# Kernel tuning notes

Hardware: AMD Instinct MI355X
Metric: run time of the kernel (lower is better)

Reference implementation:

```python
import jax, jax.numpy as jnp
import numpy as np

B, S, D = 4, 1024, 2048
H, KVH, HD = 32, 8, 64
N_REP = H // KVH  # 4
ROPE_THETA = 1000000.0


def _rope_tables(seq_len, head_dim, theta):
    inv_freq = 1.0 / (theta ** (np.arange(0, head_dim, 2, dtype=np.float32) / head_dim))
    t = np.arange(seq_len, dtype=np.float32)
    freqs = np.outer(t, inv_freq)                      # (S, HD/2)
    emb = np.concatenate([freqs, freqs], axis=-1)      # (S, HD)
    return jnp.asarray(np.cos(emb)), jnp.asarray(np.sin(emb))


def setup_inputs() -> dict:
    key = jax.random.key(0)
    kx, kq, kk, kv, ko = jax.random.split(key, 5)
    cos, sin = _rope_tables(S, HD, ROPE_THETA)
    s = 0.02
    return {
        "x": jax.random.normal(kx, (B, S, D), jnp.float32),
        "cos": cos,
        "sin": sin,
        "Wq": jax.random.normal(kq, (D, H * HD), jnp.float32) * s,
        "Wk": jax.random.normal(kk, (D, KVH * HD), jnp.float32) * s,
        "Wv": jax.random.normal(kv, (D, KVH * HD), jnp.float32) * s,
        "Wo": jax.random.normal(ko, (H * HD, D), jnp.float32) * s,
    }


def _rotate_half(t):
    t1, t2 = jnp.split(t, 2, axis=-1)
    return jnp.concatenate([-t2, t1], axis=-1)


def reference(x, cos, sin, Wq, Wk, Wv, Wo):
    # projections
    q = (x @ Wq).reshape(B, S, H, HD)      # (b, s, h, d)
    k = (x @ Wk).reshape(B, S, KVH, HD)
    v = (x @ Wv).reshape(B, S, KVH, HD)

    # RoPE: cos/sin (s, d) broadcast over heads (unsqueeze_dim=1 -> (s,1,d))
    c = cos[:, None, :]
    sn = sin[:, None, :]
    q = q * c + _rotate_half(q) * sn
    k = k * c + _rotate_half(k) * sn

    # GQA attention without physically repeating KV:
    # q grouped as (b, kvh, n_rep, s, d); repeat_kv '(h r)' maps q head g*n_rep+r -> kv head g
    qg = q.transpose(0, 2, 1, 3).reshape(B, KVH, N_REP, S, HD)
    kt = k.transpose(0, 2, 1, 3)  # (b, kvh, s, d)
    vt = v.transpose(0, 2, 1, 3)

    scale = 1.0 / jnp.sqrt(jnp.asarray(HD, x.dtype))
    scores = jnp.einsum('bgrqd,bgkd->bgrqk', qg, kt) * scale  # (b, kvh, rep, s, s)
    probs = jax.nn.softmax(scores, axis=-1)
    out = jnp.einsum('bgrqk,bgkd->bgrqd', probs, vt)           # (b, kvh, rep, s, d)

    out = out.reshape(B, H, S, HD).transpose(0, 2, 1, 3).reshape(B, S, H * HD)
    return out @ Wo
```

## Files before the change

### kernel.cpp

```cpp
#include <hip/hip_runtime.h>

typedef unsigned short u16;
typedef __attribute__((ext_vector_type(8))) __bf16 bf16x8;
typedef __attribute__((ext_vector_type(4))) _Float16 f16x4;
typedef __attribute__((ext_vector_type(8))) _Float16 f16x8;
typedef __attribute__((ext_vector_type(4))) float f32x4;

#define BB 4
#define SS 1024
#define DD 2048
#define HH 32
#define KVHN 8
#define HDIM 64

__device__ __forceinline__ u16 f2b(float f) {
    union { float f; unsigned u; } v; v.f = f;
    unsigned r = v.u + 0x7FFFu + ((v.u >> 16) & 1u);
    return (u16)(r >> 16);
}
__device__ __forceinline__ float b2f(u16 h) {
    union { unsigned u; float f; } v; v.u = ((unsigned)h) << 16; return v.f;
}

__device__ __forceinline__ f32x4 mfma16(bf16x8 a, bf16x8 b, f32x4 c) {
    return __builtin_amdgcn_mfma_f32_16x16x32_bf16(a, b, c, 0, 0, 0);
}
__device__ __forceinline__ f32x4 mfma16h(f16x8 a, f16x8 b, f32x4 c) {
    return __builtin_amdgcn_mfma_f32_16x16x32_f16(a, b, c, 0, 0, 0);
}

__device__ __forceinline__ void async_cp16(const void* g, void* l) {
    __builtin_amdgcn_global_load_lds((__attribute__((address_space(1))) void*)g,
                                     (__attribute__((address_space(3))) void*)l,
                                     16, 0, 0);
}

__device__ __forceinline__ void block_sync() {
    asm volatile("" ::: "memory");
    __builtin_amdgcn_s_barrier();
    asm volatile("" ::: "memory");
}

__device__ __forceinline__ f16x8 pack8_f16(const float* p) {
    union { unsigned u[4]; f16x8 v; } pu;
    pu.u[0] = __builtin_bit_cast(unsigned, __builtin_amdgcn_cvt_pkrtz(p[0], p[1]));
    pu.u[1] = __builtin_bit_cast(unsigned, __builtin_amdgcn_cvt_pkrtz(p[2], p[3]));
    pu.u[2] = __builtin_bit_cast(unsigned, __builtin_amdgcn_cvt_pkrtz(p[4], p[5]));
    pu.u[3] = __builtin_bit_cast(unsigned, __builtin_amdgcn_cvt_pkrtz(p[6], p[7]));
    return pu.v;
}

__global__ __launch_bounds__(256) void prep_kernel(const float* __restrict__ x,
                                                   const float* __restrict__ Wq,
                                                   const float* __restrict__ Wk,
                                                   const float* __restrict__ Wv,
                                                   const float* __restrict__ Wo,
                                                   u16* __restrict__ xb,
                                                   u16* __restrict__ Wqkvt,
                                                   u16* __restrict__ Wot) {
    __shared__ float tile[32][33];
    int z = blockIdx.z;
    int tid = threadIdx.x;
    if (z == 4) {
        int lb = blockIdx.y * 64 + blockIdx.x;
        int i = (lb * 256 + tid) * 8;
        float4 v0 = *(const float4*)(x + i);
        float4 v1 = *(const float4*)(x + i + 4);
        uint4 r;
        r.x = (unsigned)f2b(v0.x) | ((unsigned)f2b(v0.y) << 16);
        r.y = (unsigned)f2b(v0.z) | ((unsigned)f2b(v0.w) << 16);
        r.z = (unsigned)f2b(v1.x) | ((unsigned)f2b(v1.y) << 16);
        r.w = (unsigned)f2b(v1.z) | ((unsigned)f2b(v1.w) << 16);
        *(uint4*)(xb + i) = r;
        return;
    }
    const float* W = (z == 0) ? Wq : (z == 1) ? Wk : (z == 2) ? Wv : Wo;
    int N = (z == 1 || z == 2) ? 512 : 2048;
    int n_off = (z == 1) ? 2048 : (z == 2) ? 2560 : 0;
    u16* Wt = (z == 3) ? Wot : Wqkvt;
    int n0 = blockIdx.x * 32;
    if (n0 >= N) return;
    int k0 = blockIdx.y * 32;
    int nj = tid & 31;
    int ki = tid >> 5;
#pragma unroll
    for (int it = 0; it < 4; it++) {
        int kk = it * 8 + ki;
        tile[kk][nj] = W[(size_t)(k0 + kk) * N + n0 + nj];
    }
    __syncthreads();
#pragma unroll
    for (int it = 0; it < 4; it++) {
        int nn = it * 8 + ki;
        Wt[(size_t)(n0 + nn + n_off) * 2048 + k0 + nj] = f2b(tile[nj][nn]);
    }
}

__global__ __launch_bounds__(512, 2) void gemm_qkv(const u16* __restrict__ A,
                                                   const u16* __restrict__ Bt,
                                                   u16* __restrict__ C) {
    __shared__ __align__(16) u16 Ls[2][32768];
    const int tid = threadIdx.x;
    const int lane = tid & 63;
    const int w = tid >> 6;

    const int bid = blockIdx.x;
    const int xcd = bid & 7;
    const int loc = bid >> 3;
    const int mt = (xcd & 3) * 4 + (loc & 3);
    const int nt = (xcd >> 2) * 6 + (loc >> 2);
    const int m0 = mt * 256;
    const int n0 = nt * 256;

    const int wm_h = w >> 2;
    const int wn = (w & 3) * 64;
    const int lr = lane & 15;
    const int lg = lane >> 4;

    const int sr = lane >> 3;
    const int sl = (lane & 7) ^ (sr & 7);
    const u16* pA = A + (size_t)(m0 + w * 8 + sr) * 2048 + sl * 8;
    const u16* pB = Bt + (size_t)(n0 + w * 8 + sr) * 2048 + sl * 8;

#define STA(buf_, h_, kt_)                                                               \
    {                                                                                    \
        async_cp16(pA + (size_t)((h_) * 128) * 2048 + (kt_) * 64, &Ls[buf_][(h_) * 8192 + w * 512]);            \
        async_cp16(pA + (size_t)((h_) * 128 + 64) * 2048 + (kt_) * 64, &Ls[buf_][(h_) * 8192 + 4096 + w * 512]); \
    }
#define STB(buf_, h_, kt_)                                                               \
    {                                                                                    \
        async_cp16(pB + (size_t)((h_) * 128) * 2048 + (kt_) * 64, &Ls[buf_][16384 + (h_) * 8192 + w * 512]);            \
        async_cp16(pB + (size_t)((h_) * 128 + 64) * 2048 + (kt_) * 64, &Ls[buf_][16384 + (h_) * 8192 + 4096 + w * 512]); \
    }

    f32x4 acc[8][4];
    const f32x4 zero4 = {0.f, 0.f, 0.f, 0.f};
#pragma unroll
    for (int i = 0; i < 8; i++)
#pragma unroll
        for (int j = 0; j < 4; j++) acc[i][j] = zero4;

    bf16x8 af[8], b0[4], b1[4];

#define LDA(mh_, buf_)                                                                   \
    _Pragma("unroll") for (int mi = 0; mi < 4; mi++) _Pragma("unroll") for (int ks = 0; ks < 2; ks++) { \
        int rh = (mh_) * 64 + mi * 16 + lr;                                              \
        af[mi * 2 + ks] = *(const bf16x8*)(&Ls[buf_][wm_h * 8192 + rh * 64 + (((ks * 4 + lg) ^ (lr & 7)) * 8)]); \
    }
#define LDB(dst_, nh_, buf_)                                                             \
    _Pragma("unroll") for (int ni = 0; ni < 2; ni++) _Pragma("unroll") for (int ks = 0; ks < 2; ks++) { \
        int rowb = wn + (nh_) * 32 + ni * 16 + lr;                                       \
        dst_[ni * 2 + ks] = *(const bf16x8*)(&Ls[buf_][16384 + (rowb >> 7) * 8192 + (rowb & 127) * 64 + (((ks * 4 + lg) ^ (lr & 7)) * 8)]); \
    }
#define QMM(mh_, nh_, bb_)                                                               \
    __builtin_amdgcn_s_setprio(1);                                                       \
    _Pragma("unroll") for (int mi = 0; mi < 4; mi++) _Pragma("unroll") for (int ni = 0; ni < 2; ni++) { \
        acc[(mh_) * 4 + mi][(nh_) * 2 + ni] = mfma16(af[mi * 2 + 0], bb_[ni * 2 + 0], acc[(mh_) * 4 + mi][(nh_) * 2 + ni]); \
        acc[(mh_) * 4 + mi][(nh_) * 2 + ni] = mfma16(af[mi * 2 + 1], bb_[ni * 2 + 1], acc[(mh_) * 4 + mi][(nh_) * 2 + ni]); \
    }                                                                                    \
    __builtin_amdgcn_s_setprio(0);
#define WAITLDS                                                                          \
    asm volatile("s_waitcnt lgkmcnt(0)" ::: "memory");                                   \
    __builtin_amdgcn_sched_barrier(0);

    STA(0, 0, 0); STA(0, 1, 0); STB(0, 0, 0); STB(0, 1, 0);
    STB(1, 0, 1); STB(1, 1, 1);
    asm volatile("s_waitcnt vmcnt(0)" ::: "memory");
    block_sync();

#pragma unroll 1
    for (int I = 0; I < 16; ++I) {
        const int tb = 2 * I + 1;
        const int ta2 = (2 * I + 2) & 31;
        const int tb2 = (2 * I + 3) & 31;

        LDA(0, 0); LDB(b0, 0, 0);
        STA(1, 0, tb);
        block_sync(); WAITLDS;
        QMM(0, 0, b0);
        block_sync();

        LDB(b1, 1, 0);
        STA(1, 1, tb);
        block_sync(); WAITLDS;
        QMM(0, 1, b1);
        block_sync();

        LDA(1, 0);
        STB(0, 0, ta2);
        block_sync(); WAITLDS;
        QMM(1, 1, b1);
        block_sync();

        STB(0, 1, ta2);
        block_sync(); WAITLDS;
        QMM(1, 0, b0);
        asm volatile("s_waitcnt vmcnt(4)" ::: "memory");
        block_sync();

        LDA(0, 1); LDB(b0, 0, 1);
        STA(0, 0, ta2);
        block_sync(); WAITLDS;
        QMM(0, 0, b0);
        block_sync();

        LDB(b1, 1, 1);
        STA(0, 1, ta2);
        block_sync(); WAITLDS;
        QMM(0, 1, b1);
        block_sync();

        LDA(1, 1);
        STB(1, 0, tb2);
        block_sync(); WAITLDS;
        QMM(1, 1, b1);
        block_sync();

        STB(1, 1, tb2);
        block_sync(); WAITLDS;
        QMM(1, 0, b0);
        asm volatile("s_waitcnt vmcnt(4)" ::: "memory");
        block_sync();
    }
    asm volatile("s_waitcnt vmcnt(0)" ::: "memory");

    const int lq = lg * 4;
    const int wm = wm_h * 128;
#pragma unroll
    for (int mi = 0; mi < 8; mi++)
#pragma unroll
        for (int ni = 0; ni < 4; ni++)
#pragma unroll
            for (int i = 0; i < 4; i++) {
                int r = m0 + wm + mi * 16 + lq + i;
                int c = n0 + wn + ni * 16 + lr;
                C[(size_t)r * 3072 + c] = f2b(acc[mi][ni][i]);
            }
#undef STA
#undef STB
#undef LDA
#undef LDB
#undef QMM
#undef WAITLDS
}

__global__ __launch_bounds__(512, 2) void gemm_out(const u16* __restrict__ A,
                                                   const u16* __restrict__ Bt,
                                                   float* __restrict__ C) {
    __shared__ __align__(16) u16 Ls[2][24576];
    const int tid = threadIdx.x;
    const int lane = tid & 63;
    const int w = tid >> 6;

    const int bid = blockIdx.x;
    const int xcd = bid & 7;
    const int loc = bid >> 3;
    const int mt = (xcd & 3) * 4 + (loc & 3);
    const int nt = (xcd >> 2) * 8 + (loc >> 2);
    const int m0 = mt * 256;
    const int n0 = nt * 128;

    const int wm = (w >> 2) * 128;
    const int wn = (w & 3) * 32;
    const int lr = lane & 15;
    const int lg = lane >> 4;

    const int row0 = tid >> 2;
    const int g = tid & 3;
    const int sg = g ^ ((row0 >> 1) & 3);
    const u16* pA0 = A + (size_t)(m0 + row0) * 2048 + sg * 8;
    const u16* pA1 = pA0 + (size_t)128 * 2048;
    const u16* pB0 = Bt + (size_t)(n0 + row0) * 2048 + sg * 8;

#define OSTA(buf_, ks_, T_)                                                     \
    {                                                                           \
        async_cp16(pA0 + (T_) * 64 + (ks_) * 32, &Ls[buf_][(ks_) * 8192 + w * 512]);        \
        async_cp16(pA1 + (T_) * 64 + (ks_) * 32, &Ls[buf_][(ks_) * 8192 + 4096 + w * 512]); \
    }
#define OSTB(buf_, ks_, T_)                                                     \
    {                                                                           \
        async_cp16(pB0 + (T_) * 64 + (ks_) * 32, &Ls[buf_][16384 + (ks_) * 4096 + w * 512]); \
    }

    f32x4 acc[8][2];
    const f32x4 zero4 = {0.f, 0.f, 0.f, 0.f};
#pragma unroll
    for (int i = 0; i < 8; i++)
#pragma unroll
        for (int j = 0; j < 2; j++) acc[i][j] = zero4;

    bf16x8 af[8], bfr[2];

#define OLDA(ks_)                                                               \
    _Pragma("unroll") for (int mi = 0; mi < 8; mi++) {                          \
        int r_ = wm + mi * 16 + lr;                                             \
        af[mi] = *(const bf16x8*)(&Ls[cur][(ks_) * 8192 + r_ * 32 + ((lg ^ ((r_ >> 1) & 3)) * 8)]); \
    }
#define OLDB(ks_)                                                               \
    _Pragma("unroll") for (int ni = 0; ni < 2; ni++) {                          \
        int r_ = wn + ni * 16 + lr;                                             \
        bfr[ni] = *(const bf16x8*)(&Ls[cur][16384 + (ks_) * 4096 + r_ * 32 + ((lg ^ ((r_ >> 1) & 3)) * 8)]); \
    }
#define OMM                                                                     \
    __builtin_amdgcn_s_setprio(1);                                              \
    _Pragma("unroll") for (int mi = 0; mi < 8; mi++) _Pragma("unroll") for (int ni = 0; ni < 2; ni++) { \
        acc[mi][ni] = mfma16(af[mi], bfr[ni], acc[mi][ni]);                     \
    }                                                                           \
    __builtin_amdgcn_s_setprio(0);
#define OWAITMM                                                                 \
    asm volatile("s_waitcnt lgkmcnt(0)" ::: "memory");                          \
    __builtin_amdgcn_sched_barrier(0);

    OSTA(0, 0, 0); OSTB(0, 0, 0); OSTA(0, 1, 0); OSTB(0, 1, 0);
    OSTA(1, 0, 1); OSTB(1, 0, 1);
    asm volatile("s_waitcnt vmcnt(3)" ::: "memory");
    block_sync();

#pragma unroll 2
    for (int T = 0; T < 32; ++T) {
        const int cur = T & 1;
        const int oth = cur ^ 1;
        const int Tp1 = (T + 1) & 31;
        const int Tp2 = (T + 2) & 31;

        OLDA(0); OLDB(0);
        OSTA(oth, 1, Tp1); OSTB(oth, 1, Tp1);
        block_sync(); OWAITMM;
        OMM;
        block_sync();

        OLDA(1); OLDB(1);
        OSTA(cur, 0, Tp2); OSTB(cur, 0, Tp2);
        block_sync(); OWAITMM;
        OMM;
        asm volatile("s_waitcnt vmcnt(3)" ::: "memory");
        block_sync();
    }
    asm volatile("s_waitcnt vmcnt(0)" ::: "memory");

    const int lq = lg * 4;
#pragma unroll
    for (int mi = 0; mi < 8; mi++)
#pragma unroll
        for (int ni = 0; ni < 2; ni++)
#pragma unroll
            for (int i = 0; i < 4; i++) {
                int r = m0 + wm + mi * 16 + lq + i;
                int c = n0 + wn + ni * 16 + lr;
                C[(size_t)r * 2048 + c] = acc[mi][ni][i];
            }
#undef OSTA
#undef OSTB
#undef OLDA
#undef OLDB
#undef OMM
#undef OWAITMM
}

__global__ __launch_bounds__(256) void ropevt_kernel(const u16* __restrict__ QKV,
                                                     const float* __restrict__ cosT,
                                                     const float* __restrict__ sinT,
                                                     u16* __restrict__ Qh,
                                                     u16* __restrict__ Kh,
                                                     u16* __restrict__ Vt) {
    __shared__ u16 tile[64][65];
    const int bid = blockIdx.x;
    const int tid = threadIdx.x;
    if (bid < 20480) {
        const float QSC = 0.125f * 1.44269504088896f;
        int idx = bid * 256 + tid;
        int d = idx & 31;
        int t = idx >> 5;
        int hh = t % 40;
        int row = t / 40;
        int s = row & (SS - 1);
        int b = row >> 10;
        float c = cosT[s * HDIM + d];
        float sn = sinT[s * HDIM + d];
        if (hh < 32) {
            const u16* src = QKV + (size_t)row * 3072 + hh * 64 + d;
            float x1 = b2f(src[0]), x2 = b2f(src[32]);
            u16* dst = Qh + ((size_t)(b * HH + hh) * SS + s) * 64 + d;
            dst[0] = f2b((x1 * c - x2 * sn) * QSC);
            dst[32] = f2b((x2 * c + x1 * sn) * QSC);
        } else {
            int g = hh - 32;
            const u16* src = QKV + (size_t)row * 3072 + 2048 + g * 64 + d;
            float x1 = b2f(src[0]), x2 = b2f(src[32]);
            int rr = s & 7;
            int kpos = (s & ~31) + ((rr >= 4) ? 16 : 0) + ((s >> 3) & 3) * 4 + (rr & 3);
            u16* dst = Kh + ((size_t)(b * KVHN + g) * SS + kpos) * 64 + d;
            dst[0] = f2b(x1 * c - x2 * sn);
            dst[32] = f2b(x2 * c + x1 * sn);
        }
        return;
    }
    int blk = bid - 20480;
    int st = blk & 15;
    int t2 = blk >> 4;
    int g = t2 & 7;
    int b = t2 >> 3;
    int cj = tid & 63;
    int ri = tid >> 6;
    const u16* src = QKV + ((size_t)(b * SS + st * 64)) * 3072 + 2560 + g * 64;
#pragma unroll
    for (int it = 0; it < 16; it++) {
        int s_i = it * 4 + ri;
        tile[s_i][cj] = src[(size_t)s_i * 3072 + cj];
    }
    __syncthreads();
    u16* dst = Vt + ((size_t)(b * KVHN + g) * HDIM) * SS + st * 64;
#pragma unroll
    for (int it = 0; it < 16; it++) {
        int hd_i = it * 4 + ri;
        _Float16 hv = (_Float16)b2f(tile[cj][hd_i]);
        union { _Float16 h; u16 u; } cv; cv.h = hv;
        dst[(size_t)hd_i * SS + cj] = cv.u;
    }
}

__global__ __launch_bounds__(256, 2) void flash_kernel(const u16* __restrict__ Qh,
                                                       const u16* __restrict__ Kh,
                                                       const u16* __restrict__ Vt,
                                                       u16* __restrict__ Attn) {
    __shared__ __align__(16) u16 Kls[2][4096];
    __shared__ __align__(16) u16 Vls[2][4096];
    const int tid = threadIdx.x;
    const int lane = tid & 63;
    const int w = tid >> 6;
    const int bid = blockIdx.x;
    const int gbp = ((bid & 7) << 2) | ((bid >> 3) & 3);
    const int qt2 = bid >> 5;
    const int g = gbp & 7;
    const int b = gbp >> 3;
    const int h = g * 4 + w;
    const int lr = lane & 15;
    const int lg = lane >> 4;
    const int lk8 = lg * 8;
    const int lq = lg * 4;

    const u16* Qbase = Qh + ((size_t)(b * HH + h) * SS + qt2 * 64) * HDIM;
    bf16x8 qb[4][2];
#pragma unroll
    for (int j = 0; j < 4; j++) {
        qb[j][0] = *(const bf16x8*)(Qbase + (size_t)(j * 16 + lr) * HDIM + lk8);
        qb[j][1] = *(const bf16x8*)(Qbase + (size_t)(j * 16 + lr) * HDIM + 32 + lk8);
    }

    const u16* Kbase = Kh + (size_t)(b * KVHN + g) * SS * HDIM;
    const u16* Vbase = Vt + (size_t)(b * KVHN + g) * HDIM * SS;

    const int r0 = tid >> 3;
    const int c0 = tid & 7;

    const f32x4 zero4 = {0.f, 0.f, 0.f, 0.f};
    const f32x4 initS = {-4.f, -4.f, -4.f, -4.f};
    f32x4 o[4][4];
    float lsum[4] = {0.f, 0.f, 0.f, 0.f};
#pragma unroll
    for (int j = 0; j < 4; j++)
#pragma unroll
        for (int i = 0; i < 4; i++) o[j][i] = zero4;

#define STAGE(kt, p)                                                              \
    {                                                                             \
        _Pragma("unroll") for (int sh = 0; sh < 2; sh++) {                        \
            int rr = r0 + sh * 32;                                                \
            int cs = c0 ^ (rr & 7);                                              \
            async_cp16(Kbase + (size_t)((kt) + rr) * HDIM + cs * 8,               \
                       &Kls[p][sh * 2048 + w * 512]);                             \
            async_cp16(Vbase + (size_t)rr * SS + (kt) + cs * 8,                   \
                       &Vls[p][sh * 2048 + w * 512]);                             \
        }                                                                         \
    }

    STAGE(0, 0);
    __syncthreads();

    for (int t = 0; t < 16; t++) {
        const int p = t & 1;
        if (t < 15) STAGE((t + 1) * 64, p ^ 1);

#pragma unroll
        for (int c = 0; c < 2; c++) {
            f32x4 s[2][4];
#pragma unroll
            for (int halfi = 0; halfi < 2; halfi++) {
                const int R = c * 32 + halfi * 16 + lr;
                const u16* kr = &Kls[p][R * 64];
                bf16x8 kb0 = *(const bf16x8*)(kr + ((lg ^ (R & 7)) * 8));
                bf16x8 kb1 = *(const bf16x8*)(kr + (((4 + lg) ^ (R & 7)) * 8));
#pragma unroll
                for (int j = 0; j < 4; j++) {
                    f32x4 a = initS;
                    a = mfma16(kb0, qb[j][0], a);
                    a = mfma16(kb1, qb[j][1], a);
                    s[halfi][j] = a;
                }
            }

            f16x8 va[4];
#pragma unroll
            for (int hdt = 0; hdt < 4; hdt++) {
                const int R2 = hdt * 16 + lr;
                va[hdt] = *(const f16x8*)(&Vls[p][R2 * 64 + (((c * 4 + lg) ^ (R2 & 7)) * 8)]);
            }

#pragma unroll
            for (int j = 0; j < 4; j++) {
                float pv[8];
#pragma unroll
                for (int r = 0; r < 4; r++) {
                    pv[r] = __builtin_amdgcn_exp2f(s[0][j][r]);
                    pv[4 + r] = __builtin_amdgcn_exp2f(s[1][j][r]);
                }
                lsum[j] += ((pv[0] + pv[1]) + (pv[2] + pv[3])) +
                           ((pv[4] + pv[5]) + (pv[6] + pv[7]));
                f16x8 pb = pack8_f16(pv);
#pragma unroll
                for (int hdt = 0; hdt < 4; hdt++)
                    o[j][hdt] = mfma16h(va[hdt], pb, o[j][hdt]);
            }
        }
        __syncthreads();
    }

#pragma unroll
    for (int j = 0; j < 4; j++) {
        float su = lsum[j];
        su += __shfl_xor(su, 16);
        su += __shfl_xor(su, 32);
        float inv = 1.f / su;
        u16* Ob = Attn + ((size_t)(b * SS + qt2 * 64 + j * 16 + lr)) * 2048 + h * 64;
#pragma unroll
        for (int hdt = 0; hdt < 4; hdt++) {
            unsigned r0p = (unsigned)f2b(o[j][hdt][0] * inv) | ((unsigned)f2b(o[j][hdt][1] * inv) << 16);
            unsigned r1p = (unsigned)f2b(o[j][hdt][2] * inv) | ((unsigned)f2b(o[j][hdt][3] * inv) << 16);
            *(uint2*)(Ob + hdt * 16 + lq) = make_uint2(r0p, r1p);
        }
    }
}

extern "C" void kernel_launch(void* const* d_in, const int* in_sizes, int n_in,
                              void* d_out, int out_size, void* d_ws, size_t ws_size,
                              hipStream_t stream) {
    (void)in_sizes; (void)n_in; (void)out_size; (void)ws_size;
    const float* x = (const float*)d_in[0];
    const float* cosT = (const float*)d_in[1];
    const float* sinT = (const float*)d_in[2];
    const float* Wq = (const float*)d_in[3];
    const float* Wk = (const float*)d_in[4];
    const float* Wv = (const float*)d_in[5];
    const float* Wo = (const float*)d_in[6];
    float* out = (float*)d_out;

    char* ws = (char*)d_ws;
    u16* Xb    = (u16*)(ws);
    u16* Wqkvt = (u16*)(ws + 16777216);
    u16* Wot   = (u16*)(ws + 29360128);
    u16* QKV   = (u16*)(ws + 37748736);
    u16* Qh    = (u16*)(ws + 62914560);
    u16* Kh    = (u16*)(ws + 79691776);
    u16* Vt    = (u16*)(ws + 83886080);
    u16* Attn  = (u16*)(ws + 88080384);

    prep_kernel<<<dim3(64, 64, 5), 256, 0, stream>>>(x, Wq, Wk, Wv, Wo, Xb, Wqkvt, Wot);

    gemm_qkv<<<192, 512, 0, stream>>>(Xb, Wqkvt, QKV);

    ropevt_kernel<<<20992, 256, 0, stream>>>(QKV, cosT, sinT, Qh, Kh, Vt);

    flash_kernel<<<512, 256, 0, stream>>>(Qh, Kh, Vt, Attn);

    gemm_out<<<256, 512, 0, stream>>>(Attn, Wot, out);
}
```

Measured before the change: 258.5 us.

## Vectorize RoPE and weight-transpose stores, rebalance gemm_out warp tiling

The RoPE kernel now has each thread handle 8 contiguous elements with 16-byte loads and stores instead of scalar 2-byte accesses, which cuts its block count from 20480 to 2560. The weight transpose in prep packs two bf16 values into each 32-bit store. gemm_out's per-wave tile changes from 128x32 to 64x64, which lowers LDS fragment reads per MFMA (8 fragment loads for 16 MFMAs instead of 10). The goal is less memory-instruction overhead in the small kernels and better LDS reuse in the output GEMM.

```diff
diff --git a/kernel.cpp b/kernel.cpp
--- a/kernel.cpp
+++ b/kernel.cpp
@@ -89,10 +89,14 @@
         tile[kk][nj] = W[(size_t)(k0 + kk) * N + n0 + nj];
     }
     __syncthreads();
-#pragma unroll
-    for (int it = 0; it < 4; it++) {
-        int nn = it * 8 + ki;
-        Wt[(size_t)(n0 + nn + n_off) * 2048 + k0 + nj] = f2b(tile[nj][nn]);
+    int kp = tid & 15;
+    int nn8 = tid >> 4;
+#pragma unroll
+    for (int pass = 0; pass < 2; pass++) {
+        int nn = pass * 16 + nn8;
+        unsigned v = (unsigned)f2b(tile[kp * 2][nn]) |
+                     ((unsigned)f2b(tile[kp * 2 + 1][nn]) << 16);
+        *(unsigned*)&Wt[(size_t)(n0 + nn + n_off) * 2048 + k0 + kp * 2] = v;
     }
 }
 
@@ -260,8 +264,8 @@
     const int m0 = mt * 256;
     const int n0 = nt * 128;
 
-    const int wm = (w >> 2) * 128;
-    const int wn = (w & 3) * 32;
+    const int wm = (w >> 1) * 64;
+    const int wn = (w & 1) * 64;
     const int lr = lane & 15;
     const int lg = lane >> 4;
 
@@ -282,28 +286,28 @@
         async_cp16(pB0 + (T_) * 64 + (ks_) * 32, &Ls[buf_][16384 + (ks_) * 4096 + w * 512]); \
     }
 
-    f32x4 acc[8][2];
+    f32x4 acc[4][4];
     const f32x4 zero4 = {0.f, 0.f, 0.f, 0.f};
 #pragma unroll
-    for (int i = 0; i < 8; i++)
-#pragma unroll
-        for (int j = 0; j < 2; j++) acc[i][j] = zero4;
-
-    bf16x8 af[8], bfr[2];
+    for (int i = 0; i < 4; i++)
+#pragma unroll
+        for (int j = 0; j < 4; j++) acc[i][j] = zero4;
+
+    bf16x8 af[4], bfr[4];
 
 #define OLDA(ks_)                                                               \
-    _Pragma("unroll") for (int mi = 0; mi < 8; mi++) {                          \
+    _Pragma("unroll") for (int mi = 0; mi < 4; mi++) {                          \
         int r_ = wm + mi * 16 + lr;                                             \
         af[mi] = *(const bf16x8*)(&Ls[cur][(ks_) * 8192 + r_ * 32 + ((lg ^ ((r_ >> 1) & 3)) * 8)]); \
     }
 #define OLDB(ks_)                                                               \
-    _Pragma("unroll") for (int ni = 0; ni < 2; ni++) {                          \
+    _Pragma("unroll") for (int ni = 0; ni < 4; ni++) {                          \
         int r_ = wn + ni * 16 + lr;                                             \
         bfr[ni] = *(const bf16x8*)(&Ls[cur][16384 + (ks_) * 4096 + r_ * 32 + ((lg ^ ((r_ >> 1) & 3)) * 8)]); \
     }
 #define OMM                                                                     \
     __builtin_amdgcn_s_setprio(1);                                              \
-    _Pragma("unroll") for (int mi = 0; mi < 8; mi++) _Pragma("unroll") for (int ni = 0; ni < 2; ni++) { \
+    _Pragma("unroll") for (int mi = 0; mi < 4; mi++) _Pragma("unroll") for (int ni = 0; ni < 4; ni++) { \
         acc[mi][ni] = mfma16(af[mi], bfr[ni], acc[mi][ni]);                     \
     }                                                                           \
     __builtin_amdgcn_s_setprio(0);
@@ -340,9 +344,9 @@
 
     const int lq = lg * 4;
 #pragma unroll
-    for (int mi = 0; mi < 8; mi++)
-#pragma unroll
-        for (int ni = 0; ni < 2; ni++)
+    for (int mi = 0; mi < 4; mi++)
+#pragma unroll
+        for (int ni = 0; ni < 4; ni++)
 #pragma unroll
             for (int i = 0; i < 4; i++) {
                 int r = m0 + wm + mi * 16 + lq + i;
@@ -366,36 +370,57 @@
     __shared__ u16 tile[64][65];
     const int bid = blockIdx.x;
     const int tid = threadIdx.x;
-    if (bid < 20480) {
+    if (bid < 2560) {
         const float QSC = 0.125f * 1.44269504088896f;
         int idx = bid * 256 + tid;
-        int d = idx & 31;
-        int t = idx >> 5;
+        int t = idx >> 2;
+        int dq = (idx & 3) * 8;
         int hh = t % 40;
         int row = t / 40;
         int s = row & (SS - 1);
         int b = row >> 10;
-        float c = cosT[s * HDIM + d];
-        float sn = sinT[s * HDIM + d];
+        float4 c0 = *(const float4*)(cosT + s * HDIM + dq);
+        float4 c1 = *(const float4*)(cosT + s * HDIM + dq + 4);
+        float4 s0 = *(const float4*)(sinT + s * HDIM + dq);
+        float4 s1 = *(const float4*)(sinT + s * HDIM + dq + 4);
+        float cv[8] = {c0.x, c0.y, c0.z, c0.w, c1.x, c1.y, c1.z, c1.w};
+        float sv[8] = {s0.x, s0.y, s0.z, s0.w, s1.x, s1.y, s1.z, s1.w};
+        const u16* src;
+        u16* dst;
+        float scale;
         if (hh < 32) {
-            const u16* src = QKV + (size_t)row * 3072 + hh * 64 + d;
-            float x1 = b2f(src[0]), x2 = b2f(src[32]);
-            u16* dst = Qh + ((size_t)(b * HH + hh) * SS + s) * 64 + d;
-            dst[0] = f2b((x1 * c - x2 * sn) * QSC);
-            dst[32] = f2b((x2 * c + x1 * sn) * QSC);
+            src = QKV + (size_t)row * 3072 + hh * 64 + dq;
+            dst = Qh + ((size_t)(b * HH + hh) * SS + s) * 64 + dq;
+            scale = QSC;
         } else {
             int g = hh - 32;
-            const u16* src = QKV + (size_t)row * 3072 + 2048 + g * 64 + d;
-            float x1 = b2f(src[0]), x2 = b2f(src[32]);
+            src = QKV + (size_t)row * 3072 + 2048 + g * 64 + dq;
             int rr = s & 7;
             int kpos = (s & ~31) + ((rr >= 4) ? 16 : 0) + ((s >> 3) & 3) * 4 + (rr & 3);
-            u16* dst = Kh + ((size_t)(b * KVHN + g) * SS + kpos) * 64 + d;
-            dst[0] = f2b(x1 * c - x2 * sn);
-            dst[32] = f2b(x2 * c + x1 * sn);
+            dst = Kh + ((size_t)(b * KVHN + g) * SS + kpos) * 64 + dq;
+            scale = 1.0f;
         }
+        uint4 x1u = *(const uint4*)(src);
+        uint4 x2u = *(const uint4*)(src + 32);
+        const u16* x1p = (const u16*)&x1u;
+        const u16* x2p = (const u16*)&x2u;
+        unsigned o1[4], o2[4];
+#pragma unroll
+        for (int i = 0; i < 4; i++) {
+            float a0 = b2f(x1p[2 * i]),     b0v = b2f(x2p[2 * i]);
+            float a1 = b2f(x1p[2 * i + 1]), b1v = b2f(x2p[2 * i + 1]);
+            float r00 = (a0 * cv[2 * i] - b0v * sv[2 * i]) * scale;
+            float r01 = (a1 * cv[2 * i + 1] - b1v * sv[2 * i + 1]) * scale;
+            float r10 = (b0v * cv[2 * i] + a0 * sv[2 * i]) * scale;
+            float r11 = (b1v * cv[2 * i + 1] + a1 * sv[2 * i + 1]) * scale;
+            o1[i] = (unsigned)f2b(r00) | ((unsigned)f2b(r01) << 16);
+            o2[i] = (unsigned)f2b(r10) | ((unsigned)f2b(r11) << 16);
+        }
+        *(uint4*)(dst) = make_uint4(o1[0], o1[1], o1[2], o1[3]);
+        *(uint4*)(dst + 32) = make_uint4(o2[0], o2[1], o2[2], o2[3]);
         return;
     }
-    int blk = bid - 20480;
+    int blk = bid - 2560;
     int st = blk & 15;
     int t2 = blk >> 4;
     int g = t2 & 7;
@@ -414,8 +439,8 @@
     for (int it = 0; it < 16; it++) {
         int hd_i = it * 4 + ri;
         _Float16 hv = (_Float16)b2f(tile[cj][hd_i]);
-        union { _Float16 h; u16 u; } cv; cv.h = hv;
-        dst[(size_t)hd_i * SS + cj] = cv.u;
+        union { _Float16 h; u16 u; } cv2; cv2.h = hv;
+        dst[(size_t)hd_i * SS + cj] = cv2.u;
     }
 }
 
@@ -568,7 +593,7 @@
 
     gemm_qkv<<<192, 512, 0, stream>>>(Xb, Wqkvt, QKV);
 
-    ropevt_kernel<<<20992, 256, 0, stream>>>(QKV, cosT, sinT, Qh, Kh, Vt);
+    ropevt_kernel<<<3072, 256, 0, stream>>>(QKV, cosT, sinT, Qh, Kh, Vt);
 
     flash_kernel<<<512, 256, 0, stream>>>(Qh, Kh, Vt, Attn);
 
```

Result: no change. 260.4 us (+0.7%).
